# Optimization experiments

Measured on AMD Instinct MI355X. Metric: run time of the kernel, lower is better.

The kernel has to match this reference:

```python
import jax, jax.numpy as jnp
import numpy as np

N, M, G = 50000, 400000, 128   # nodes, undirected edges, graphs
FN, FE, L, O = 128, 32, 128, 128
MAX_LV = 3


def setup_inputs() -> dict:
    rng = np.random.default_rng(0)
    key = jax.random.key(0)
    ks = jax.random.split(key, 12)
    # random multigraph without self-loops; directed edges interleaved so that
    # edge 2i = (u->v) and edge 2i+1 = (v->u) (reverse edge = e ^ 1)
    u = rng.integers(0, N, size=M)
    v = (u + 1 + rng.integers(0, N - 1, size=M)) % N
    src = np.empty(2 * M, dtype=np.int32)
    dst = np.empty(2 * M, dtype=np.int32)
    src[0::2], src[1::2] = u, v
    dst[0::2], dst[1::2] = v, u
    graph_ids = np.sort(rng.integers(0, G, size=N)).astype(np.int32)

    def lin(k, fan_in, fan_out):
        return jax.random.normal(k, (fan_in, fan_out), jnp.float32) / np.sqrt(fan_in)

    return {
        "node_feat": jax.random.normal(ks[0], (N, FN), jnp.float32),
        "edge_feat": jax.random.normal(ks[1], (2 * M, FE), jnp.float32),
        "w_n2l_W": lin(ks[2], FN, L), "w_n2l_b": jnp.zeros((L,), jnp.float32),
        "w_e2l_W": lin(ks[3], FE, L), "w_e2l_b": jnp.zeros((L,), jnp.float32),
        "conv_W": lin(ks[4], L, L),   "conv_b": jnp.zeros((L,), jnp.float32),
        "out_W": lin(ks[5], L, O),    "out_b": jnp.zeros((O,), jnp.float32),
        "edge_src": jnp.asarray(src),
        "edge_dst": jnp.asarray(dst),
        "graph_ids": jnp.asarray(graph_ids),
        "num_graphs": G,
    }


def _swap_reverse(msgs):
    # message of the reverse directed edge: pairs are interleaved (2i, 2i+1)
    E, D = msgs.shape
    return msgs.reshape(E // 2, 2, D)[:, ::-1, :].reshape(E, D)


def reference(node_feat, edge_feat, w_n2l_W, w_n2l_b, w_e2l_W, w_e2l_b,
              conv_W, conv_b, out_W, out_b, edge_src, edge_dst, graph_ids,
              num_graphs):
    n_nodes = node_feat.shape[0]
    # n2e_sp @ (W_n node_feat): gather source-node linear features onto edges
    input_node_linear = node_feat @ w_n2l_W + w_n2l_b          # [N, L]
    input_message = input_node_linear[edge_src]                # [E, L]
    input_message = input_message + (edge_feat @ w_e2l_W + w_e2l_b)
    cur = jax.nn.relu(input_message)                           # input_potential
    for _ in range(MAX_LV):
        # e2e_sp @ cur: sum of messages into src node, minus reverse edge
        node_agg = jax.ops.segment_sum(cur, edge_dst, num_segments=n_nodes)
        e2epool = node_agg[edge_src] - _swap_reverse(cur)      # [E, L]
        cur = jax.nn.relu(e2epool @ conv_W + conv_b + input_message)
    # e2n_sp @ cur: sum edge messages into destination nodes
    e2npool = jax.ops.segment_sum(cur, edge_dst, num_segments=n_nodes)
    hidden_msg = jax.nn.relu(e2npool)                          # [N, L]
    reluact = jax.nn.relu(hidden_msg @ out_W + out_b)          # [N, O]
    # subg_sp @ reluact: pool nodes per graph
    y = jax.ops.segment_sum(reluact, graph_ids, num_segments=num_graphs)
    return jax.nn.relu(y)                                      # [G, O]
```

## Files before the change

kernel.cpp:

```cpp
#include <hip/hip_runtime.h>
#include <hip/hip_bf16.h>
#include <stdint.h>

typedef __attribute__((ext_vector_type(8))) short short8;
typedef __attribute__((ext_vector_type(4))) float f32x4;

__device__ __forceinline__ float b2f(ushort u) {
  union { uint32_t i; float f; } v; v.i = ((uint32_t)u) << 16; return v.f;
}
__device__ __forceinline__ ushort f2b(float f) {
  union { float f; uint32_t i; } v; v.f = f;
  uint32_t x = v.i;
  uint32_t r = x + 0x7FFFu + ((x >> 16) & 1u);
  return (ushort)(r >> 16);
}
__device__ __forceinline__ uint pk2(float lo, float hi) {
  return (uint)f2b(lo) | ((uint)f2b(hi) << 16);
}
__device__ __forceinline__ float lo2f(uint v) { return b2f((ushort)(v & 0xFFFFu)); }
__device__ __forceinline__ float hi2f(uint v) { return b2f((ushort)(v >> 16)); }

__device__ __forceinline__ uint4 pkf8(float4 a, float4 b) {
  uint4 o;
  o.x = pk2(a.x, a.y); o.y = pk2(a.z, a.w);
  o.z = pk2(b.x, b.y); o.w = pk2(b.z, b.w);
  return o;
}
__device__ __forceinline__ uint sub2(uint a, uint b) {
  return pk2(lo2f(a) - lo2f(b), hi2f(a) - hi2f(b));
}
__device__ __forceinline__ uint4 sub8(uint4 a, uint4 b) {
  uint4 o; o.x = sub2(a.x,b.x); o.y = sub2(a.y,b.y); o.z = sub2(a.z,b.z); o.w = sub2(a.w,b.w); return o;
}
__device__ __forceinline__ uint addrelu2(uint a, uint b) {
  return pk2(fmaxf(lo2f(a) + lo2f(b), 0.f), fmaxf(hi2f(a) + hi2f(b), 0.f));
}
__device__ __forceinline__ uint4 addrelu8(uint4 a, uint4 b) {
  uint4 o; o.x = addrelu2(a.x,b.x); o.y = addrelu2(a.y,b.y);
  o.z = addrelu2(a.z,b.z); o.w = addrelu2(a.w,b.w); return o;
}
__device__ __forceinline__ uint relu2(uint v) {
  uint lo = (v & 0x8000u) ? 0u : (v & 0xFFFFu);
  uint hi = (v & 0x80000000u) ? 0u : (v & 0xFFFF0000u);
  return lo | hi;
}
__device__ __forceinline__ uint4 relu8(uint4 v) {
  uint4 o; o.x = relu2(v.x); o.y = relu2(v.y); o.z = relu2(v.z); o.w = relu2(v.w); return o;
}

__global__ void zero_ints(int* __restrict__ p, int n) {
  int i = blockIdx.x * blockDim.x + threadIdx.x;
  if (i < n) p[i] = 0;
}

__global__ void prep_weights(const float* __restrict__ wn, const float* __restrict__ we,
                             const float* __restrict__ cw, const float* __restrict__ ow,
                             const float* __restrict__ cb, const float* __restrict__ be,
                             ushort* __restrict__ wnT, ushort* __restrict__ weT,
                             ushort* __restrict__ cweT, ushort* __restrict__ owT,
                             float* __restrict__ cbe) {
  int i = blockIdx.x * blockDim.x + threadIdx.x;
  if (i < 16384) {
    int n = i >> 7, k = i & 127; wnT[n*128+k] = f2b(wn[k*128+n]);
  } else if (i < 32768) {
    int j = i - 16384; int n = j >> 7, k = j & 127; owT[n*128+k] = f2b(ow[k*128+n]);
  } else if (i < 53248) {
    int j = i - 32768;
    int n = j / 160, k = j % 160;
    cweT[n*160+k] = (k < 128) ? f2b(cw[k*128+n]) : f2b(we[(k-128)*128+n]);
  } else if (i < 57344) {
    int j = i - 53248; int n = j >> 5, k = j & 31; weT[n*32+k] = f2b(we[k*128+n]);
  } else if (i < 57472) {
    int j = i - 57344; cbe[j] = cb[j] + be[j];
  }
}

__global__ void count_dst(const int* __restrict__ dst, int* __restrict__ counts, int E) {
  for (int i = blockIdx.x * blockDim.x + threadIdx.x; i < E; i += gridDim.x * blockDim.x)
    atomicAdd(&counts[dst[i]], 1);
}
__global__ __launch_bounds__(1024) void scan_offsets(
    const int* __restrict__ counts, int* __restrict__ off,
    int* __restrict__ cursor, int N) {
  __shared__ int part[1024];
  int t = threadIdx.x;
  int chunk = (N + 1023) >> 10;
  int lo = t * chunk, hi = min(lo + chunk, N);
  int s = 0;
  for (int i = lo; i < hi; ++i) s += counts[i];
  part[t] = s;
  __syncthreads();
  for (int d = 1; d < 1024; d <<= 1) {
    int v = (t >= d) ? part[t - d] : 0;
    __syncthreads();
    part[t] += v;
    __syncthreads();
  }
  int run = (t > 0) ? part[t - 1] : 0;
  for (int i = lo; i < hi; ++i) {
    off[i] = run; cursor[i] = run; run += counts[i];
  }
  if (t == 1023) off[N] = part[1023];
}
__global__ void fill_csr(const int* __restrict__ dst, int* __restrict__ cursor,
                         int* __restrict__ eids, int E) {
  for (int i = blockIdx.x * blockDim.x + threadIdx.x; i < E; i += gridDim.x * blockDim.x) {
    int p = atomicAdd(&cursor[dst[i]], 1);
    eids[p] = i;
  }
}

__global__ __launch_bounds__(256) void node_linear(
    const float* __restrict__ nf, const ushort* __restrict__ wnT,
    const float* __restrict__ bn, ushort* __restrict__ inl, int N) {
  __shared__ ushort Als[64][136];
  __shared__ ushort Bls[128][136];
  int tid = threadIdx.x;
  int n0 = blockIdx.x * 64;
  {
    int row = tid >> 1, h = tid & 1;
    const uint4* gp = (const uint4*)(wnT + row*128 + h*64);
    uint4* lp = (uint4*)&Bls[row][h*64];
    #pragma unroll
    for (int i = 0; i < 8; ++i) lp[i] = gp[i];
  }
  {
    int r = tid >> 2, q = tid & 3;
    int n = n0 + r;
    uint4* lp = (uint4*)&Als[r][q*32];
    if (n < N) {
      const float4* fp = (const float4*)(nf + (size_t)n*128 + q*32);
      #pragma unroll
      for (int i = 0; i < 4; ++i) lp[i] = pkf8(fp[2*i], fp[2*i+1]);
    } else {
      uint4 z = {0,0,0,0};
      #pragma unroll
      for (int i = 0; i < 4; ++i) lp[i] = z;
    }
  }
  __syncthreads();
  int l = tid & 63, w = tid >> 6, quad = l >> 4, mr = l & 15;
  f32x4 acc[8];
  #pragma unroll
  for (int nt = 0; nt < 8; ++nt) acc[nt] = (f32x4){0.f,0.f,0.f,0.f};
  #pragma unroll
  for (int kk = 0; kk < 4; ++kk) {
    short8 a = *(const short8*)&Als[w*16 + mr][kk*32 + quad*8];
    #pragma unroll
    for (int nt = 0; nt < 8; ++nt) {
      short8 b = *(const short8*)&Bls[nt*16 + mr][kk*32 + quad*8];
      acc[nt] = __builtin_amdgcn_mfma_f32_16x16x32_bf16(a, b, acc[nt], 0, 0, 0);
    }
  }
  #pragma unroll
  for (int nt = 0; nt < 8; ++nt) {
    int col = nt*16 + mr;
    float bias = bn[col];
    #pragma unroll
    for (int rg = 0; rg < 4; ++rg) {
      int n = n0 + w*16 + quad*4 + rg;
      if (n < N) inl[(size_t)n*128 + col] = f2b(acc[nt][rg] + bias);
    }
  }
}

__global__ __launch_bounds__(256) void edge_init(
    const float* __restrict__ ef, const ushort* __restrict__ weT,
    const float* __restrict__ be, const int* __restrict__ esrc,
    const ushort* __restrict__ inl, ushort* __restrict__ cur, int E) {
  __shared__ ushort Als[64][40];
  __shared__ ushort Cls[64][136];
  int tid = threadIdx.x;
  int e0 = blockIdx.x * 64;
  int l = tid & 63, w = tid >> 6, quad = l >> 4, mr = l & 15;
  int r = tid >> 2, q = tid & 3;

  short8 bfrag[2];
  #pragma unroll
  for (int nt = 0; nt < 2; ++nt)
    bfrag[nt] = *(const short8*)(weT + (size_t)(w*32 + nt*16 + mr)*32 + quad*8);

  {
    const float4* fp = (const float4*)(ef + (size_t)(e0 + r)*32 + q*8);
    *(uint4*)&Als[r][q*8] = pkf8(fp[0], fp[1]);
  }
  __syncthreads();

  int col0 = w*32 + mr, col1 = w*32 + 16 + mr;
  float bias0 = be[col0], bias1 = be[col1];
  #pragma unroll
  for (int m = 0; m < 4; ++m) {
    short8 a = *(const short8*)&Als[m*16 + mr][quad*8];
    f32x4 zero = (f32x4){0.f,0.f,0.f,0.f};
    f32x4 acc0 = __builtin_amdgcn_mfma_f32_16x16x32_bf16(a, bfrag[0], zero, 0, 0, 0);
    f32x4 acc1 = __builtin_amdgcn_mfma_f32_16x16x32_bf16(a, bfrag[1], zero, 0, 0, 0);
    #pragma unroll
    for (int rg = 0; rg < 4; ++rg) {
      int row = m*16 + quad*4 + rg;
      Cls[row][col0] = f2b(acc0[rg] + bias0);
      Cls[row][col1] = f2b(acc1[rg] + bias1);
    }
  }
  __syncthreads();

  {
    int e = e0 + r;
    int s = esrc[e];
    const uint4* cl = (const uint4*)&Cls[r][q*32];
    const uint4* ip = (const uint4*)(inl + (size_t)s*128 + q*32);
    uint4* op = (uint4*)(cur + (size_t)e*128 + q*32);
    #pragma unroll
    for (int i = 0; i < 4; ++i) op[i] = addrelu8(cl[i], ip[i]);
  }
}

__global__ __launch_bounds__(256) void segsum(
    const ushort* __restrict__ cur, const int* __restrict__ off,
    const int* __restrict__ eids, ushort* __restrict__ nagg, int N) {
  int w = threadIdx.x >> 6, l = threadIdx.x & 63;
  int n = blockIdx.x * 4 + w;
  if (n >= N) return;
  int i = off[n], end = off[n + 1];
  float s0 = 0.f, s1 = 0.f;
  for (; i + 8 <= end; i += 8) {
    int e[8]; uint v[8];
    #pragma unroll
    for (int j = 0; j < 8; ++j) e[j] = eids[i + j];
    #pragma unroll
    for (int j = 0; j < 8; ++j) v[j] = *(const uint*)(cur + (size_t)e[j]*128 + 2*l);
    #pragma unroll
    for (int j = 0; j < 8; ++j) { s0 += lo2f(v[j]); s1 += hi2f(v[j]); }
  }
  for (; i < end; ++i) {
    int ea = eids[i];
    uint va = *(const uint*)(cur + (size_t)ea*128 + 2*l);
    s0 += lo2f(va); s1 += hi2f(va);
  }
  *(uint*)(nagg + (size_t)n*128 + 2*l) = pk2(s0, s1);
}

__global__ __launch_bounds__(256) void conv_step(
    ushort* __restrict__ cur, const ushort* __restrict__ nagg,
    const ushort* __restrict__ inl, const float* __restrict__ ef,
    const ushort* __restrict__ cweT, const float* __restrict__ cbe,
    const int* __restrict__ esrc, int E) {
  __shared__ ushort Als[64][168];
  __shared__ ushort Cls[64][136];
  int tid = threadIdx.x;
  int e0 = blockIdx.x * 64;
  int l = tid & 63, w = tid >> 6, quad = l >> 4, mr = l & 15;
  int r = tid >> 2, q = tid & 3;

  short8 bfrag[2][5];
  #pragma unroll
  for (int nt = 0; nt < 2; ++nt) {
    const ushort* bp = cweT + (size_t)(w*32 + nt*16 + mr) * 160;
    #pragma unroll
    for (int kk = 0; kk < 5; ++kk)
      bfrag[nt][kk] = *(const short8*)(bp + kk*32 + quad*8);
  }

  {
    int e = e0 + r;
    int s = esrc[e];
    const uint4* cp = (const uint4*)(cur + (size_t)(e ^ 1)*128 + q*32);
    const uint4* np = (const uint4*)(nagg + (size_t)s*128 + q*32);
    uint4* lp = (uint4*)&Als[r][q*32];
    #pragma unroll
    for (int i = 0; i < 4; ++i) lp[i] = sub8(np[i], cp[i]);
    const float4* fp = (const float4*)(ef + (size_t)e*32 + q*8);
    *(uint4*)&Als[r][128 + q*8] = pkf8(fp[0], fp[1]);
  }
  __syncthreads();

  int col0 = w*32 + mr, col1 = w*32 + 16 + mr;
  float bias0 = cbe[col0], bias1 = cbe[col1];
  #pragma unroll
  for (int m = 0; m < 4; ++m) {
    f32x4 acc0 = (f32x4){0.f,0.f,0.f,0.f};
    f32x4 acc1 = (f32x4){0.f,0.f,0.f,0.f};
    #pragma unroll
    for (int kk = 0; kk < 5; ++kk) {
      short8 a = *(const short8*)&Als[m*16 + mr][kk*32 + quad*8];
      acc0 = __builtin_amdgcn_mfma_f32_16x16x32_bf16(a, bfrag[0][kk], acc0, 0, 0, 0);
      acc1 = __builtin_amdgcn_mfma_f32_16x16x32_bf16(a, bfrag[1][kk], acc1, 0, 0, 0);
    }
    #pragma unroll
    for (int rg = 0; rg < 4; ++rg) {
      int row = m*16 + quad*4 + rg;
      Cls[row][col0] = f2b(acc0[rg] + bias0);
      Cls[row][col1] = f2b(acc1[rg] + bias1);
    }
  }
  __syncthreads();

  {
    int e = e0 + r;
    int s = esrc[e];
    const uint4* cl = (const uint4*)&Cls[r][q*32];
    const uint4* ip = (const uint4*)(inl + (size_t)s*128 + q*32);
    uint4* op = (uint4*)(cur + (size_t)e*128 + q*32);
    #pragma unroll
    for (int i = 0; i < 4; ++i) op[i] = addrelu8(cl[i], ip[i]);
  }
}

__global__ __launch_bounds__(256) void out_linear(
    const ushort* __restrict__ nagg, const ushort* __restrict__ owT,
    const float* __restrict__ ob, ushort* __restrict__ ract, int N) {
  __shared__ ushort Als[64][136];
  __shared__ ushort Bls[128][136];
  int tid = threadIdx.x;
  int n0 = blockIdx.x * 64;
  {
    int row = tid >> 1, h = tid & 1;
    const uint4* gp = (const uint4*)(owT + row*128 + h*64);
    uint4* lp = (uint4*)&Bls[row][h*64];
    #pragma unroll
    for (int i = 0; i < 8; ++i) lp[i] = gp[i];
  }
  {
    int r = tid >> 2, q = tid & 3;
    int n = n0 + r;
    uint4* lp = (uint4*)&Als[r][q*32];
    if (n < N) {
      const uint4* gp = (const uint4*)(nagg + (size_t)n*128 + q*32);
      #pragma unroll
      for (int i = 0; i < 4; ++i) lp[i] = relu8(gp[i]);
    } else {
      uint4 z = {0,0,0,0};
      #pragma unroll
      for (int i = 0; i < 4; ++i) lp[i] = z;
    }
  }
  __syncthreads();
  int l = tid & 63, w = tid >> 6, quad = l >> 4, mr = l & 15;
  f32x4 acc[8];
  #pragma unroll
  for (int nt = 0; nt < 8; ++nt) acc[nt] = (f32x4){0.f,0.f,0.f,0.f};
  #pragma unroll
  for (int kk = 0; kk < 4; ++kk) {
    short8 a = *(const short8*)&Als[w*16 + mr][kk*32 + quad*8];
    #pragma unroll
    for (int nt = 0; nt < 8; ++nt) {
      short8 b = *(const short8*)&Bls[nt*16 + mr][kk*32 + quad*8];
      acc[nt] = __builtin_amdgcn_mfma_f32_16x16x32_bf16(a, b, acc[nt], 0, 0, 0);
    }
  }
  #pragma unroll
  for (int nt = 0; nt < 8; ++nt) {
    int col = nt*16 + mr;
    float bias = ob[col];
    #pragma unroll
    for (int rg = 0; rg < 4; ++rg) {
      int n = n0 + w*16 + quad*4 + rg;
      if (n < N) ract[(size_t)n*128 + col] = f2b(fmaxf(acc[nt][rg] + bias, 0.f));
    }
  }
}

__global__ void graph_offsets(const int* __restrict__ gids, int* __restrict__ goff,
                              int N, int G) {
  int i = blockIdx.x * blockDim.x + threadIdx.x;
  if (i > N) return;
  int pg = (i == 0) ? -1 : gids[i - 1];
  int cg = (i == N) ? G : gids[i];
  for (int g = pg + 1; g <= cg; ++g) goff[g] = i;
}

__global__ __launch_bounds__(256) void graph_pool(
    const ushort* __restrict__ ract, const int* __restrict__ goff,
    float* __restrict__ out, int G) {
  __shared__ float red0[256];
  __shared__ float red1[256];
  int g = blockIdx.x;
  int t = threadIdx.x;
  int c2 = t & 63, rp = t >> 6;
  int beg = goff[g], end = goff[g + 1];
  float s0 = 0.f, s1 = 0.f;
  for (int n = beg + rp; n < end; n += 4) {
    uint v = *(const uint*)(ract + (size_t)n*128 + 2*c2);
    s0 += lo2f(v); s1 += hi2f(v);
  }
  red0[t] = s0; red1[t] = s1;
  __syncthreads();
  if (rp == 0) {
    float v0 = red0[c2] + red0[c2 + 64] + red0[c2 + 128] + red0[c2 + 192];
    float v1 = red1[c2] + red1[c2 + 64] + red1[c2 + 128] + red1[c2 + 192];
    float2 o; o.x = fmaxf(v0, 0.f); o.y = fmaxf(v1, 0.f);
    *(float2*)(out + (size_t)g*128 + 2*c2) = o;
  }
}

extern "C" void kernel_launch(void* const* d_in, const int* in_sizes, int n_in,
                              void* d_out, int out_size, void* d_ws, size_t ws_size,
                              hipStream_t stream) {
  const float* node_feat = (const float*)d_in[0];
  const float* edge_feat = (const float*)d_in[1];
  const float* wn = (const float*)d_in[2];
  const float* bn = (const float*)d_in[3];
  const float* we = (const float*)d_in[4];
  const float* be = (const float*)d_in[5];
  const float* cw = (const float*)d_in[6];
  const float* cb = (const float*)d_in[7];
  const float* ow = (const float*)d_in[8];
  const float* ob = (const float*)d_in[9];
  const int* esrc = (const int*)d_in[10];
  const int* edst = (const int*)d_in[11];
  const int* gids = (const int*)d_in[12];
  int N = in_sizes[0] / 128;
  int E = in_sizes[10];
  int G = out_size / 128;
  float* out = (float*)d_out;

  char* p = (char*)d_ws;
  auto alloc = [&](size_t bytes) {
    char* r = p;
    p += (bytes + 255) & ~(size_t)255;
    return r;
  };
  ushort* cur     = (ushort*)alloc((size_t)E * 128 * 2);
  ushort* inl     = (ushort*)alloc((size_t)N * 128 * 2);
  ushort* nagg    = (ushort*)alloc((size_t)N * 128 * 2);
  int*    eids    = (int*)   alloc((size_t)E * 4);
  int*    counts  = (int*)   alloc((size_t)N * 4);
  int*    off     = (int*)   alloc((size_t)(N + 1) * 4);
  int*    cursor  = (int*)   alloc((size_t)N * 4);
  int*    goff    = (int*)   alloc((size_t)(G + 1) * 4);
  ushort* wnT     = (ushort*)alloc(128 * 128 * 2);
  ushort* weT     = (ushort*)alloc(128 * 32 * 2);
  ushort* cweT    = (ushort*)alloc(128 * 160 * 2);
  ushort* owT     = (ushort*)alloc(128 * 128 * 2);
  float*  cbe     = (float*) alloc(128 * 4);
  ushort* ract    = inl;
  (void)ws_size; (void)n_in;

  zero_ints<<<(N + 255) / 256, 256, 0, stream>>>(counts, N);
  prep_weights<<<225, 256, 0, stream>>>(wn, we, cw, ow, cb, be, wnT, weT, cweT, owT, cbe);
  count_dst<<<1024, 256, 0, stream>>>(edst, counts, E);
  scan_offsets<<<1, 1024, 0, stream>>>(counts, off, cursor, N);
  fill_csr<<<1024, 256, 0, stream>>>(edst, cursor, eids, E);

  node_linear<<<(N + 63) / 64, 256, 0, stream>>>(node_feat, wnT, bn, inl, N);
  edge_init<<<E / 64, 256, 0, stream>>>(edge_feat, weT, be, esrc, inl, cur, E);

  for (int it = 0; it < 3; ++it) {
    segsum<<<(N + 3) / 4, 256, 0, stream>>>(cur, off, eids, nagg, N);
    conv_step<<<E / 64, 256, 0, stream>>>(cur, nagg, inl, edge_feat, cweT, cbe, esrc, E);
  }
  segsum<<<(N + 3) / 4, 256, 0, stream>>>(cur, off, eids, nagg, N);
  out_linear<<<(N + 63) / 64, 256, 0, stream>>>(nagg, owT, ob, ract, N);
  graph_offsets<<<(N + 256) / 256, 256, 0, stream>>>(gids, goff, N, G);
  graph_pool<<<G, 256, 0, stream>>>(ract, goff, out, G);
}
```

Before: 1.179 ms.

## Cache bf16 edge features, reuse LDS tile, use hardware bf16 pack

During edge_init the fp32 edge features are converted to bf16 once and written to a workspace buffer, so each conv_step reads half the bytes and skips the conversion. conv_step drops its separate output LDS tile by writing results back into the input tile after an extra barrier, keeping accumulators in registers; this lowers LDS use per block and may allow higher occupancy. The software bf16 rounding is replaced by the hardware packed convert builtin when the compiler provides it. The cost is an extra workspace buffer plus one extra write in edge_init, and more live accumulator registers.

```diff
diff --git a/kernel.cpp b/kernel.cpp
--- a/kernel.cpp
+++ b/kernel.cpp
@@ -5,17 +5,35 @@
 typedef __attribute__((ext_vector_type(8))) short short8;
 typedef __attribute__((ext_vector_type(4))) float f32x4;
 
+#if defined(__has_builtin)
+#if __has_builtin(__builtin_amdgcn_cvt_pk_bf16_f32)
+#define HAVE_PK_BF16 1
+#endif
+#endif
+
 __device__ __forceinline__ float b2f(ushort u) {
   union { uint32_t i; float f; } v; v.i = ((uint32_t)u) << 16; return v.f;
 }
-__device__ __forceinline__ ushort f2b(float f) {
+__device__ __forceinline__ ushort f2b_sw(float f) {
   union { float f; uint32_t i; } v; v.f = f;
   uint32_t x = v.i;
   uint32_t r = x + 0x7FFFu + ((x >> 16) & 1u);
   return (ushort)(r >> 16);
 }
 __device__ __forceinline__ uint pk2(float lo, float hi) {
-  return (uint)f2b(lo) | ((uint)f2b(hi) << 16);
+#ifdef HAVE_PK_BF16
+  auto r = __builtin_amdgcn_cvt_pk_bf16_f32(lo, hi);
+  union { decltype(r) v; uint u; } c; c.v = r; return c.u;
+#else
+  return (uint)f2b_sw(lo) | ((uint)f2b_sw(hi) << 16);
+#endif
+}
+__device__ __forceinline__ ushort f2b(float f) {
+#ifdef HAVE_PK_BF16
+  return (ushort)(pk2(f, 0.f) & 0xFFFFu);
+#else
+  return f2b_sw(f);
+#endif
 }
 __device__ __forceinline__ float lo2f(uint v) { return b2f((ushort)(v & 0xFFFFu)); }
 __device__ __forceinline__ float hi2f(uint v) { return b2f((ushort)(v >> 16)); }
@@ -167,7 +185,8 @@
 __global__ __launch_bounds__(256) void edge_init(
     const float* __restrict__ ef, const ushort* __restrict__ weT,
     const float* __restrict__ be, const int* __restrict__ esrc,
-    const ushort* __restrict__ inl, ushort* __restrict__ cur, int E) {
+    const ushort* __restrict__ inl, ushort* __restrict__ cur,
+    ushort* __restrict__ efb, int E) {
   __shared__ ushort Als[64][40];
   __shared__ ushort Cls[64][136];
   int tid = threadIdx.x;
@@ -182,7 +201,9 @@
 
   {
     const float4* fp = (const float4*)(ef + (size_t)(e0 + r)*32 + q*8);
-    *(uint4*)&Als[r][q*8] = pkf8(fp[0], fp[1]);
+    uint4 pk = pkf8(fp[0], fp[1]);
+    *(uint4*)&Als[r][q*8] = pk;
+    if (efb) *(uint4*)(efb + (size_t)(e0 + r)*32 + q*8) = pk;
   }
   __syncthreads();
 
@@ -241,11 +262,10 @@
 
 __global__ __launch_bounds__(256) void conv_step(
     ushort* __restrict__ cur, const ushort* __restrict__ nagg,
-    const ushort* __restrict__ inl, const float* __restrict__ ef,
-    const ushort* __restrict__ cweT, const float* __restrict__ cbe,
-    const int* __restrict__ esrc, int E) {
+    const ushort* __restrict__ inl, const ushort* __restrict__ efb,
+    const float* __restrict__ ef, const ushort* __restrict__ cweT,
+    const float* __restrict__ cbe, const int* __restrict__ esrc, int E) {
   __shared__ ushort Als[64][168];
-  __shared__ ushort Cls[64][136];
   int tid = threadIdx.x;
   int e0 = blockIdx.x * 64;
   int l = tid & 63, w = tid >> 6, quad = l >> 4, mr = l & 15;
@@ -268,28 +288,38 @@
     uint4* lp = (uint4*)&Als[r][q*32];
     #pragma unroll
     for (int i = 0; i < 4; ++i) lp[i] = sub8(np[i], cp[i]);
-    const float4* fp = (const float4*)(ef + (size_t)e*32 + q*8);
-    *(uint4*)&Als[r][128 + q*8] = pkf8(fp[0], fp[1]);
+    if (efb) {
+      *(uint4*)&Als[r][128 + q*8] = *(const uint4*)(efb + (size_t)e*32 + q*8);
+    } else {
+      const float4* fp = (const float4*)(ef + (size_t)e*32 + q*8);
+      *(uint4*)&Als[r][128 + q*8] = pkf8(fp[0], fp[1]);
+    }
   }
   __syncthreads();
 
   int col0 = w*32 + mr, col1 = w*32 + 16 + mr;
   float bias0 = cbe[col0], bias1 = cbe[col1];
+  f32x4 acc0[4], acc1[4];
   #pragma unroll
   for (int m = 0; m < 4; ++m) {
-    f32x4 acc0 = (f32x4){0.f,0.f,0.f,0.f};
-    f32x4 acc1 = (f32x4){0.f,0.f,0.f,0.f};
+    acc0[m] = (f32x4){0.f,0.f,0.f,0.f};
+    acc1[m] = (f32x4){0.f,0.f,0.f,0.f};
     #pragma unroll
     for (int kk = 0; kk < 5; ++kk) {
       short8 a = *(const short8*)&Als[m*16 + mr][kk*32 + quad*8];
-      acc0 = __builtin_amdgcn_mfma_f32_16x16x32_bf16(a, bfrag[0][kk], acc0, 0, 0, 0);
-      acc1 = __builtin_amdgcn_mfma_f32_16x16x32_bf16(a, bfrag[1][kk], acc1, 0, 0, 0);
-    }
+      acc0[m] = __builtin_amdgcn_mfma_f32_16x16x32_bf16(a, bfrag[0][kk], acc0[m], 0, 0, 0);
+      acc1[m] = __builtin_amdgcn_mfma_f32_16x16x32_bf16(a, bfrag[1][kk], acc1[m], 0, 0, 0);
+    }
+  }
+  __syncthreads();
+
+  #pragma unroll
+  for (int m = 0; m < 4; ++m) {
     #pragma unroll
     for (int rg = 0; rg < 4; ++rg) {
       int row = m*16 + quad*4 + rg;
-      Cls[row][col0] = f2b(acc0[rg] + bias0);
-      Cls[row][col1] = f2b(acc1[rg] + bias1);
+      Als[row][col0] = f2b(acc0[m][rg] + bias0);
+      Als[row][col1] = f2b(acc1[m][rg] + bias1);
     }
   }
   __syncthreads();
@@ -297,7 +327,7 @@
   {
     int e = e0 + r;
     int s = esrc[e];
-    const uint4* cl = (const uint4*)&Cls[r][q*32];
+    const uint4* cl = (const uint4*)&Als[r][q*32];
     const uint4* ip = (const uint4*)(inl + (size_t)s*128 + q*32);
     uint4* op = (uint4*)(cur + (size_t)e*128 + q*32);
     #pragma unroll
@@ -432,8 +462,10 @@
   ushort* cweT    = (ushort*)alloc(128 * 160 * 2);
   ushort* owT     = (ushort*)alloc(128 * 128 * 2);
   float*  cbe     = (float*) alloc(128 * 4);
+  ushort* efb     = (ushort*)alloc((size_t)E * 32 * 2);
+  if ((size_t)(p - (char*)d_ws) > ws_size) efb = nullptr;
   ushort* ract    = inl;
-  (void)ws_size; (void)n_in;
+  (void)n_in;
 
   zero_ints<<<(N + 255) / 256, 256, 0, stream>>>(counts, N);
   prep_weights<<<225, 256, 0, stream>>>(wn, we, cw, ow, cb, be, wnT, weT, cweT, owT, cbe);
@@ -442,11 +474,11 @@
   fill_csr<<<1024, 256, 0, stream>>>(edst, cursor, eids, E);
 
   node_linear<<<(N + 63) / 64, 256, 0, stream>>>(node_feat, wnT, bn, inl, N);
-  edge_init<<<E / 64, 256, 0, stream>>>(edge_feat, weT, be, esrc, inl, cur, E);
+  edge_init<<<E / 64, 256, 0, stream>>>(edge_feat, weT, be, esrc, inl, cur, efb, E);
 
   for (int it = 0; it < 3; ++it) {
     segsum<<<(N + 3) / 4, 256, 0, stream>>>(cur, off, eids, nagg, N);
-    conv_step<<<E / 64, 256, 0, stream>>>(cur, nagg, inl, edge_feat, cweT, cbe, esrc, E);
+    conv_step<<<E / 64, 256, 0, stream>>>(cur, nagg, inl, efb, edge_feat, cweT, cbe, esrc, E);
   }
   segsum<<<(N + 3) / 4, 256, 0, stream>>>(cur, off, eids, nagg, N);
   out_linear<<<(N + 63) / 64, 256, 0, stream>>>(nagg, owT, ob, ract, N);
```

Result: no change. 1.188 ms (+0.8%).
